# Kernel optimization log

Measured on AMD Instinct MI355X. Metric: run time of the kernel, lower is better.

The kernel has to match this reference:

```python
import jax, jax.numpy as jnp
import numpy as np

B, S, D, H = 2, 2048, 1024, 16
HD = D // H  # head dim = 64


def setup_inputs() -> dict:
    key = jax.random.key(0)
    ks = jax.random.split(key, 5)
    scale = 0.02
    x = jax.random.normal(ks[0], (B, S, D), dtype=jnp.float32)
    Wqkv = jax.random.normal(ks[1], (D, 3 * D), dtype=jnp.float32) * scale
    bqkv = jnp.zeros((3 * D,), dtype=jnp.float32)
    Wproj = jax.random.normal(ks[2], (D, D), dtype=jnp.float32) * scale
    bproj = jnp.zeros((D,), dtype=jnp.float32)
    return {"x": x, "Wqkv": Wqkv, "bqkv": bqkv, "Wproj": Wproj, "bproj": bproj}


def reference(x, Wqkv, bqkv, Wproj, bproj):
    # fused QKV projection
    qkv = x @ Wqkv + bqkv                      # [B, S, 3D]
    q, k, v = jnp.split(qkv, 3, axis=-1)       # each [B, S, D]
    # split heads -> [B, H, S, HD]
    def heads(t):
        return t.reshape(B, S, H, HD).transpose(0, 2, 1, 3)
    q, k, v = heads(q), heads(k), heads(v)
    # scaled dot-product attention with causal mask (GPT-2 style)
    scores = jnp.einsum('bhqd,bhkd->bhqk', q, k) / jnp.sqrt(jnp.float32(HD))
    causal = jnp.tril(jnp.ones((S, S), dtype=bool))
    scores = jnp.where(causal, scores, jnp.finfo(scores.dtype).min)
    attn = jax.nn.softmax(scores, axis=-1)      # [B, H, S, S]
    out = jnp.einsum('bhqk,bhkd->bhqd', attn, v)  # [B, H, S, HD]
    out = out.transpose(0, 2, 1, 3).reshape(B, S, D)
    return out @ Wproj + bproj
```

## Files before the change

kernel.cpp:

```cpp
#include <hip/hip_runtime.h>
#include <hip/hip_bf16.h>


typedef __attribute__((ext_vector_type(8))) short short8;
typedef __attribute__((ext_vector_type(4))) float float4v;

#define S_LEN 2048
#define NHEAD 16
#define HDIM  64
#define DMODEL 1024

__device__ __forceinline__ unsigned short f2bf(float f) {
    union { float f; unsigned u; } v; v.f = f;
    unsigned r = v.u + 0x7FFF + ((v.u >> 16) & 1);
    return (unsigned short)(r >> 16);
}

__device__ __forceinline__ unsigned fbits_rn(float f) {
    union { float f; unsigned u; } v; v.f = f;
    return v.u + 0x8000u;
}

__device__ __forceinline__ void async16(const void* g, const void* l) {
    __builtin_amdgcn_global_load_lds(
        (const __attribute__((address_space(1))) unsigned int*)g,
        (__attribute__((address_space(3))) unsigned int*)l, 16, 0, 0);
}

__global__ void f32_to_bf16_v4(const float4* __restrict__ in,
                               ushort4* __restrict__ out, int n4) {
    int i = blockIdx.x * blockDim.x + threadIdx.x;
    if (i < n4) {
        float4 v = in[i];
        ushort4 o;
        o.x = f2bf(v.x); o.y = f2bf(v.y); o.z = f2bf(v.z); o.w = f2bf(v.w);
        out[i] = o;
    }
}

__global__ __launch_bounds__(256) void w_transpose_bf16(
    const float* __restrict__ Wqkv, const float* __restrict__ Wproj,
    unsigned short* __restrict__ outQ, unsigned short* __restrict__ outP) {
    __shared__ float t[64][65];
    const float* in; unsigned short* out; int N, bxl;
    if (blockIdx.x < 48) { in = Wqkv;  out = outQ; N = 3072; bxl = blockIdx.x; }
    else                 { in = Wproj; out = outP; N = 1024; bxl = blockIdx.x - 48; }
    const int K = 1024;
    const int kb = blockIdx.y * 64, nb = bxl * 64;
    const int tid = threadIdx.x;
    const int r0 = tid >> 4, c0 = (tid & 15) * 4;
#pragma unroll
    for (int g = 0; g < 4; g++) {
        float4 v = *(const float4*)(in + (size_t)(kb + g * 16 + r0) * N + nb + c0);
        t[g * 16 + r0][c0 + 0] = v.x; t[g * 16 + r0][c0 + 1] = v.y;
        t[g * 16 + r0][c0 + 2] = v.z; t[g * 16 + r0][c0 + 3] = v.w;
    }
    __syncthreads();
#pragma unroll
    for (int g = 0; g < 4; g++) {
        int n = g * 16 + r0;
        ushort4 o;
        o.x = f2bf(t[c0 + 0][n]); o.y = f2bf(t[c0 + 1][n]);
        o.z = f2bf(t[c0 + 2][n]); o.w = f2bf(t[c0 + 3][n]);
        *(ushort4*)(out + (size_t)(nb + n) * K + kb + c0) = o;
    }
}

__global__ __launch_bounds__(256) void v_pack(
    const unsigned short* __restrict__ V, unsigned short* __restrict__ Vp) {
    __shared__ unsigned short t[64 * 68];
    const int bh = blockIdx.y;
    const int c0 = blockIdx.x;
    const int s0 = c0 * 64;
    const int tid = threadIdx.x;
    const int r = tid >> 2, c4 = tid & 3;
    const size_t base = (size_t)bh * S_LEN * HDIM;
    union { uint4 v[2]; unsigned short u[16]; } d;
    const unsigned short* src = V + base + (size_t)(s0 + r) * HDIM + c4 * 16;
    d.v[0] = *(const uint4*)(src);
    d.v[1] = *(const uint4*)(src + 8);
#pragma unroll
    for (int j = 0; j < 16; j++) t[r * 68 + c4 * 16 + j] = d.u[j];
    __syncthreads();
    unsigned short* outb = Vp + ((size_t)(bh * 32 + c0)) * 4096;
#pragma unroll
    for (int pi = 0; pi < 2; pi++) {
        const int p = tid * 2 + pi;
        const int lane = p & 63, kk = (p >> 6) & 1, nt = p >> 7;
        const int q = lane >> 4, l = lane & 15;
        union { ushort4 v[2]; unsigned short u[8]; } w;
#pragma unroll
        for (int j = 0; j < 8; j++) {
            const int key = (kk * 2 + (j >> 2)) * 16 + q * 4 + (j & 3);
            w.u[j] = t[key * 68 + nt * 16 + l];
        }
        unsigned short* po = outb + ((nt * 2 + kk) * 64 + lane) * 8;
        *(ushort4*)(po) = w.v[0];
        *(ushort4*)(po + 4) = w.v[1];
    }
}

#define QSCALE 0.18033688f

__global__ __launch_bounds__(256) void gemm_qkv_kernel(
    const unsigned short* __restrict__ A,
    const unsigned short* __restrict__ Bt,
    const float* __restrict__ bias,
    unsigned short* __restrict__ out_q,
    unsigned short* __restrict__ out_kp,
    unsigned short* __restrict__ out_v,
    int M, int N, int K)
{
    __shared__ unsigned short smem[128 * 132];
    unsigned short* As = smem;
    unsigned short* Bs = smem + 8192;

    const int tid  = threadIdx.x;
    const int lane = tid & 63;
    const int wave = tid >> 6;
    const int quad = lane >> 4;
    const int l16  = lane & 15;

    const int m0 = blockIdx.y * 128;
    const int n0 = blockIdx.x * 128;
    const int wm = (wave >> 1) * 64;
    const int wn = (wave & 1) * 64;

    float4v acc[4][4];
#pragma unroll
    for (int i = 0; i < 4; i++)
#pragma unroll
        for (int j = 0; j < 4; j++) acc[i][j] = (float4v){0.f, 0.f, 0.f, 0.f};

    const int srow = lane >> 2;
    const int scol = (lane & 3) * 8;

    for (int k0 = 0; k0 < K; k0 += 64) {
        __syncthreads();
#pragma unroll
        for (int kk = 0; kk < 2; kk++)
#pragma unroll
            for (int it = 0; it < 2; it++) {
                const int rg = it * 64 + wave * 16;
                async16(A  + (size_t)(m0 + rg + srow) * K + k0 + kk * 32 + scol,
                        (const char*)(As + kk * 4096) + rg * 64);
                async16(Bt + (size_t)(n0 + rg + srow) * K + k0 + kk * 32 + scol,
                        (const char*)(Bs + kk * 4096) + rg * 64);
            }
        __syncthreads();

#pragma unroll
        for (int kk = 0; kk < 2; kk++) {
            short8 af[4], bf[4];
#pragma unroll
            for (int mt = 0; mt < 4; mt++)
                af[mt] = *(const short8*)(As + kk * 4096
                                          + (wm + mt * 16 + l16) * 32 + quad * 8);
#pragma unroll
            for (int nt = 0; nt < 4; nt++)
                bf[nt] = *(const short8*)(Bs + kk * 4096
                                          + (wn + nt * 16 + l16) * 32 + quad * 8);
#pragma unroll
            for (int mt = 0; mt < 4; mt++)
#pragma unroll
                for (int nt = 0; nt < 4; nt++)
                    acc[mt][nt] = __builtin_amdgcn_mfma_f32_16x16x32_bf16(
                        af[mt], bf[nt], acc[mt][nt], 0, 0, 0);
        }
    }

    __syncthreads();
#pragma unroll
    for (int nt = 0; nt < 4; nt++) {
        const int col = n0 + wn + nt * 16 + l16;
        const float sc = ((col >> 10) == 0) ? QSCALE : 1.0f;
        const float bia = bias[col] * sc;
        const int cold = (wn + nt * 16 + l16) >> 1;
#pragma unroll
        for (int mt = 0; mt < 4; mt++)
#pragma unroll
            for (int r = 0; r < 4; r++) {
                unsigned fb = fbits_rn(acc[mt][nt][r] * sc + bia);
                unsigned fbp = (unsigned)__shfl_xor((int)fb, 1, 64);
                unsigned pd = (l16 & 1)
                    ? __builtin_amdgcn_perm(fb, fbp, 0x07060302)
                    : __builtin_amdgcn_perm(fbp, fb, 0x07060302);
                const int rowl = wm + mt * 16 + quad * 4 + r;
                *((unsigned*)smem + rowl * 66 + cold) = pd;
            }
    }
    __syncthreads();

#pragma unroll
    for (int ps = 0; ps < 8; ps++) {
        const int row = ps * 16 + (tid >> 4);
        const int pc  = tid & 15;
        const int col0 = pc * 8;
        const int cb = n0 + (col0 >> 6) * 64;
        const int part = cb >> 10;
        const int hh = (cb & 1023) >> 6;
        const int gr = m0 + row;
        const int b = gr >> 11, s = gr & 2047;
        const size_t bhI = (size_t)(b * NHEAD + hh);
        const unsigned short* pl = smem + row * 132 + col0;
        uint2 a = *(const uint2*)(pl);
        uint2 bb = *(const uint2*)(pl + 4);
        uint4 w; w.x = a.x; w.y = a.y; w.z = bb.x; w.w = bb.y;
        unsigned short* po;
        if (part == 1) {
            const int hd = col0 & 63;
            const int h = hd >> 5, q = (hd >> 3) & 3;
            po = out_kp + ((((bhI * 32 + (s >> 6)) * 4 + ((s >> 4) & 3)) * 2 + h)
                           * 64 + q * 16 + (s & 15)) * 8;
        } else {
            unsigned short* dst = (part == 0) ? out_q : out_v;
            po = dst + (bhI * S_LEN + s) * HDIM + (col0 & 63);
        }
        *(uint4*)po = w;
    }
}

__global__ __launch_bounds__(256) void gemm_proj_kernel(
    const unsigned short* __restrict__ A,
    const unsigned short* __restrict__ Bt,
    const float* __restrict__ bias,
    float* __restrict__ out_f,
    int M, int N, int K)
{
    __shared__ unsigned short smem[12288];
    unsigned short* As = smem;
    unsigned short* Bs = smem + 4096;

    const int tid  = threadIdx.x;
    const int lane = tid & 63;
    const int wave = tid >> 6;
    const int quad = lane >> 4;
    const int l16  = lane & 15;

    const int m0 = blockIdx.y * 64;
    const int n0 = blockIdx.x * 128;
    const int wm = (wave >> 1) * 32;
    const int wn = (wave & 1) * 64;

    float4v acc[2][4];
#pragma unroll
    for (int i = 0; i < 2; i++)
#pragma unroll
        for (int j = 0; j < 4; j++) acc[i][j] = (float4v){0.f, 0.f, 0.f, 0.f};

    const int srow = lane >> 2;
    const int scol = (lane & 3) * 8;

    for (int k0 = 0; k0 < K; k0 += 64) {
        __syncthreads();
#pragma unroll
        for (int kk = 0; kk < 2; kk++) {
            async16(A + (size_t)(m0 + wave * 16 + srow) * K + k0 + kk * 32 + scol,
                    (const char*)(As + kk * 2048) + wave * 1024);
#pragma unroll
            for (int it = 0; it < 2; it++) {
                const int rg = it * 64 + wave * 16;
                async16(Bt + (size_t)(n0 + rg + srow) * K + k0 + kk * 32 + scol,
                        (const char*)(Bs + kk * 4096) + rg * 64);
            }
        }
        __syncthreads();

#pragma unroll
        for (int kk = 0; kk < 2; kk++) {
            short8 af[2], bf[4];
#pragma unroll
            for (int mt = 0; mt < 2; mt++)
                af[mt] = *(const short8*)(As + kk * 2048
                                          + (wm + mt * 16 + l16) * 32 + quad * 8);
#pragma unroll
            for (int nt = 0; nt < 4; nt++)
                bf[nt] = *(const short8*)(Bs + kk * 4096
                                          + (wn + nt * 16 + l16) * 32 + quad * 8);
#pragma unroll
            for (int mt = 0; mt < 2; mt++)
#pragma unroll
                for (int nt = 0; nt < 4; nt++)
                    acc[mt][nt] = __builtin_amdgcn_mfma_f32_16x16x32_bf16(
                        af[mt], bf[nt], acc[mt][nt], 0, 0, 0);
        }
    }

#pragma unroll
    for (int nt = 0; nt < 4; nt++) {
        const int col = n0 + wn + nt * 16 + l16;
        const float bia = bias[col];
#pragma unroll
        for (int mt = 0; mt < 2; mt++) {
            const int rowb = m0 + wm + mt * 16 + quad * 4;
#pragma unroll
            for (int r = 0; r < 4; r++)
                out_f[(size_t)(rowb + r) * N + col] = acc[mt][nt][r] + bia;
        }
    }
}

__global__ __launch_bounds__(256, 2) void attn7_kernel(
    const unsigned short* __restrict__ Q,
    const unsigned short* __restrict__ Kp,
    const unsigned short* __restrict__ Vp,
    unsigned short* __restrict__ ctx)
{
    __shared__ unsigned short lds[2][8192];

    const int tid  = threadIdx.x;
    const int lane = tid & 63;
    const int wave = tid >> 6;
    const int quad = lane >> 4;
    const int l16  = lane & 15;

    const int bx = blockIdx.x;
    const int bh = bx & 31;
    const int g  = bx >> 5;
    const int qb = (g < 8) ? (15 - g) : (g - 8);
    const int q0w = qb * 128 + wave * 32;
    const int nch = 2 * qb + 2;

    const size_t baseQ = (size_t)bh * S_LEN * HDIM;
    const unsigned short* kb_ = Kp + (size_t)bh * 32 * 4096;
    const unsigned short* vb_ = Vp + (size_t)bh * 32 * 4096;

    short8 qf[2][2];
#pragma unroll
    for (int qt = 0; qt < 2; qt++)
#pragma unroll
        for (int h = 0; h < 2; h++)
            qf[qt][h] = *(const short8*)(Q + baseQ
                                         + (size_t)(q0w + qt * 16 + l16) * HDIM
                                         + h * 32 + quad * 8);

    float4v o[2][4];
#pragma unroll
    for (int qt = 0; qt < 2; qt++)
#pragma unroll
        for (int nt = 0; nt < 4; nt++) o[qt][nt] = (float4v){0.f, 0.f, 0.f, 0.f};
    float lsa[2][4];
#pragma unroll
    for (int qt = 0; qt < 2; qt++)
#pragma unroll
        for (int kt = 0; kt < 4; kt++) lsa[qt][kt] = 0.f;

    {
        unsigned short* sb = &lds[0][0];
        async16(kb_ + tid * 8,        sb + wave * 512);
        async16(kb_ + 2048 + tid * 8, sb + 2048 + wave * 512);
        async16(vb_ + tid * 8,        sb + 4096 + wave * 512);
        async16(vb_ + 2048 + tid * 8, sb + 6144 + wave * 512);
    }

    for (int c = 0; c < nch; c++) {
        __syncthreads();
        const unsigned short* lb = &lds[c & 1][0];
        const int kb0 = c * 64;
        const bool wactive = (kb0 <= q0w + 31);

        short8 kf[4][2];
        if (wactive) {
#pragma unroll
            for (int kt = 0; kt < 4; kt++)
#pragma unroll
                for (int h = 0; h < 2; h++)
                    kf[kt][h] = *(const short8*)(lb
                                                 + ((kt * 2 + h) * 64 + lane) * 8);
        }

        if (c + 1 < nch) {
            const unsigned short* kc = kb_ + (size_t)(c + 1) * 4096;
            const unsigned short* vc = vb_ + (size_t)(c + 1) * 4096;
            unsigned short* sb = &lds[(c + 1) & 1][0];
            async16(kc + tid * 8,        sb + wave * 512);
            async16(kc + 2048 + tid * 8, sb + 2048 + wave * 512);
            async16(vc + tid * 8,        sb + 4096 + wave * 512);
            async16(vc + 2048 + tid * 8, sb + 6144 + wave * 512);
        }

        if (wactive) {
            float4v st[2][4];
#pragma unroll
            for (int qt = 0; qt < 2; qt++)
#pragma unroll
                for (int kt = 0; kt < 4; kt++) {
                    st[qt][kt] = __builtin_amdgcn_mfma_f32_16x16x32_bf16(
                        kf[kt][0], qf[qt][0], (float4v){0.f, 0.f, 0.f, 0.f},
                        0, 0, 0);
                    st[qt][kt] = __builtin_amdgcn_mfma_f32_16x16x32_bf16(
                        kf[kt][1], qf[qt][1], st[qt][kt], 0, 0, 0);
                }

            short8 vf[4][2];
#pragma unroll
            for (int nt = 0; nt < 4; nt++)
#pragma unroll
                for (int kk = 0; kk < 2; kk++)
                    vf[nt][kk] = *(const short8*)(lb + 4096
                                                  + ((nt * 2 + kk) * 64 + lane) * 8);

#pragma unroll
            for (int qt = 0; qt < 2; qt++) {
                const int q0t = q0w + qt * 16;
                const bool needmask = (kb0 + 63 > q0t);
                const int qpos = q0t + l16;
                float p[4][4];
#pragma unroll
                for (int kt = 0; kt < 4; kt++)
#pragma unroll
                    for (int r = 0; r < 4; r++) {
                        float x = st[qt][kt][r];
                        if (needmask) {
                            int kpos = kb0 + kt * 16 + quad * 4 + r;
                            x = (kpos <= qpos) ? x : -1e30f;
                        }
                        p[kt][r] = __builtin_amdgcn_exp2f(x);
                        lsa[qt][kt] += p[kt][r];
                    }

                unsigned pk[4][2];
#pragma unroll
                for (int kt = 0; kt < 4; kt++)
#pragma unroll
                    for (int j = 0; j < 2; j++)
                        pk[kt][j] = __builtin_amdgcn_perm(
                            fbits_rn(p[kt][2 * j + 1]), fbits_rn(p[kt][2 * j]),
                            0x07060302);
                union { unsigned u[4]; short8 s; } pf[2];
#pragma unroll
                for (int kk = 0; kk < 2; kk++)
#pragma unroll
                    for (int pp = 0; pp < 4; pp++)
                        pf[kk].u[pp] = pk[kk * 2 + (pp >> 1)][pp & 1];

#pragma unroll
                for (int nt = 0; nt < 4; nt++) {
                    o[qt][nt] = __builtin_amdgcn_mfma_f32_16x16x32_bf16(
                        pf[0].s, vf[nt][0], o[qt][nt], 0, 0, 0);
                    o[qt][nt] = __builtin_amdgcn_mfma_f32_16x16x32_bf16(
                        pf[1].s, vf[nt][1], o[qt][nt], 0, 0, 0);
                }
            }
        }
    }

    const int b = bh >> 4, h = bh & 15;
#pragma unroll
    for (int qt = 0; qt < 2; qt++) {
        float l = (lsa[qt][0] + lsa[qt][1]) + (lsa[qt][2] + lsa[qt][3]);
        l += __shfl_xor(l, 16, 64);
        l += __shfl_xor(l, 32, 64);
        const float linv = 1.f / l;
        float lr[4];
#pragma unroll
        for (int r = 0; r < 4; r++) lr[r] = __shfl(linv, quad * 4 + r, 64);
#pragma unroll
        for (int r = 0; r < 4; r++) {
            const int s = q0w + qt * 16 + quad * 4 + r;
            const size_t off = ((size_t)(b * S_LEN + s)) * DMODEL + h * HDIM;
#pragma unroll
            for (int nt = 0; nt < 4; nt++)
                ctx[off + nt * 16 + l16] = f2bf(o[qt][nt][r] * lr[r]);
        }
    }
}

extern "C" void kernel_launch(void* const* d_in, const int* in_sizes, int n_in,
                              void* d_out, int out_size, void* d_ws, size_t ws_size,
                              hipStream_t stream) {
    const float* x     = (const float*)d_in[0];
    const float* Wqkv  = (const float*)d_in[1];
    const float* bqkv  = (const float*)d_in[2];
    const float* Wproj = (const float*)d_in[3];
    const float* bproj = (const float*)d_in[4];
    float* out = (float*)d_out;

    const int M  = 2 * S_LEN;
    const int N1 = 3 * DMODEL;
    const int K  = DMODEL;

    unsigned short* x_bf    = (unsigned short*)d_ws;
    unsigned short* wqkv_t  = x_bf   + (size_t)M * K;
    unsigned short* wproj_t = wqkv_t + (size_t)K * N1;
    unsigned short* q_bf    = wproj_t + (size_t)K * DMODEL;
    unsigned short* kp_bf   = q_bf   + (size_t)M * DMODEL;
    unsigned short* v_bf    = kp_bf  + (size_t)M * DMODEL;
    unsigned short* ctx_bf  = v_bf   + (size_t)M * DMODEL;
    unsigned short* vp_bf   = x_bf;

    {
        int n4 = (M * K) / 4;
        f32_to_bf16_v4<<<n4 / 256, 256, 0, stream>>>((const float4*)x,
                                                     (ushort4*)x_bf, n4);
    }
    {
        dim3 g(64, 16);
        w_transpose_bf16<<<g, 256, 0, stream>>>(Wqkv, Wproj, wqkv_t, wproj_t);
    }

    dim3 g1(N1 / 128, M / 128);
    gemm_qkv_kernel<<<g1, 256, 0, stream>>>(x_bf, wqkv_t, bqkv,
                                            q_bf, kp_bf, v_bf, M, N1, K);

    {
        dim3 g(S_LEN / 64, 2 * NHEAD);
        v_pack<<<g, 256, 0, stream>>>(v_bf, vp_bf);
    }

    attn7_kernel<<<512, 256, 0, stream>>>(q_bf, kp_bf, vp_bf, ctx_bf);

    dim3 g3(DMODEL / 128, M / 64);
    gemm_proj_kernel<<<g3, 256, 0, stream>>>(ctx_bf, wproj_t, bproj, out,
                                             M, DMODEL, K);
}
```

Measured before the change: 184.1 us.

## Halve attention block to 64 queries with 2 waves and 1024 blocks

The attention kernel now uses 128-thread blocks covering 64 query rows instead of 256 threads covering 128, and launches twice as many blocks. Each K/V chunk is loaded by fewer threads in four iterations, and the per-wave causal skip is removed because every wave now works on every chunk up to the diagonal. This cuts the idle waves and load imbalance along the causal diagonal and spreads work across more blocks. In exchange, each K/V tile is reused by only two waves, so total LDS fill traffic roughly doubles.

```diff
diff --git a/kernel.cpp b/kernel.cpp
--- a/kernel.cpp
+++ b/kernel.cpp
@@ -300,7 +300,7 @@
     }
 }
 
-__global__ __launch_bounds__(256, 2) void attn7_kernel(
+__global__ __launch_bounds__(128, 2) void attn8_kernel(
     const unsigned short* __restrict__ Q,
     const unsigned short* __restrict__ Kp,
     const unsigned short* __restrict__ Vp,
@@ -317,9 +317,13 @@
     const int bx = blockIdx.x;
     const int bh = bx & 31;
     const int g  = bx >> 5;
-    const int qb = (g < 8) ? (15 - g) : (g - 8);
-    const int q0w = qb * 128 + wave * 32;
-    const int nch = 2 * qb + 2;
+    const int g0 = g & 7, gt = g >> 3;
+    const int qb = (gt == 0) ? (31 - g0)
+                 : (gt == 1) ? (16 + g0)
+                 : (gt == 2) ? (15 - g0)
+                 :             g0;
+    const int q0w = qb * 64 + wave * 32;
+    const int nch = qb + 1;
 
     const size_t baseQ = (size_t)bh * S_LEN * HDIM;
     const unsigned short* kb_ = Kp + (size_t)bh * 32 * 4096;
@@ -347,100 +351,100 @@
 
     {
         unsigned short* sb = &lds[0][0];
-        async16(kb_ + tid * 8,        sb + wave * 512);
-        async16(kb_ + 2048 + tid * 8, sb + 2048 + wave * 512);
-        async16(vb_ + tid * 8,        sb + 4096 + wave * 512);
-        async16(vb_ + 2048 + tid * 8, sb + 6144 + wave * 512);
+#pragma unroll
+        for (int i = 0; i < 4; i++) {
+            async16(kb_ + (size_t)(i * 128 + tid) * 8,
+                    sb + (i * 128 + wave * 64) * 8);
+            async16(vb_ + (size_t)(i * 128 + tid) * 8,
+                    sb + 4096 + (i * 128 + wave * 64) * 8);
+        }
     }
 
     for (int c = 0; c < nch; c++) {
         __syncthreads();
         const unsigned short* lb = &lds[c & 1][0];
         const int kb0 = c * 64;
-        const bool wactive = (kb0 <= q0w + 31);
 
         short8 kf[4][2];
-        if (wactive) {
-#pragma unroll
-            for (int kt = 0; kt < 4; kt++)
-#pragma unroll
-                for (int h = 0; h < 2; h++)
-                    kf[kt][h] = *(const short8*)(lb
-                                                 + ((kt * 2 + h) * 64 + lane) * 8);
-        }
+#pragma unroll
+        for (int kt = 0; kt < 4; kt++)
+#pragma unroll
+            for (int h = 0; h < 2; h++)
+                kf[kt][h] = *(const short8*)(lb + ((kt * 2 + h) * 64 + lane) * 8);
 
         if (c + 1 < nch) {
             const unsigned short* kc = kb_ + (size_t)(c + 1) * 4096;
             const unsigned short* vc = vb_ + (size_t)(c + 1) * 4096;
             unsigned short* sb = &lds[(c + 1) & 1][0];
-            async16(kc + tid * 8,        sb + wave * 512);
-            async16(kc + 2048 + tid * 8, sb + 2048 + wave * 512);
-            async16(vc + tid * 8,        sb + 4096 + wave * 512);
-            async16(vc + 2048 + tid * 8, sb + 6144 + wave * 512);
-        }
-
-        if (wactive) {
-            float4v st[2][4];
-#pragma unroll
-            for (int qt = 0; qt < 2; qt++)
-#pragma unroll
-                for (int kt = 0; kt < 4; kt++) {
-                    st[qt][kt] = __builtin_amdgcn_mfma_f32_16x16x32_bf16(
-                        kf[kt][0], qf[qt][0], (float4v){0.f, 0.f, 0.f, 0.f},
-                        0, 0, 0);
-                    st[qt][kt] = __builtin_amdgcn_mfma_f32_16x16x32_bf16(
-                        kf[kt][1], qf[qt][1], st[qt][kt], 0, 0, 0);
+#pragma unroll
+            for (int i = 0; i < 4; i++) {
+                async16(kc + (size_t)(i * 128 + tid) * 8,
+                        sb + (i * 128 + wave * 64) * 8);
+                async16(vc + (size_t)(i * 128 + tid) * 8,
+                        sb + 4096 + (i * 128 + wave * 64) * 8);
+            }
+        }
+
+        float4v st[2][4];
+#pragma unroll
+        for (int qt = 0; qt < 2; qt++)
+#pragma unroll
+            for (int kt = 0; kt < 4; kt++) {
+                st[qt][kt] = __builtin_amdgcn_mfma_f32_16x16x32_bf16(
+                    kf[kt][0], qf[qt][0], (float4v){0.f, 0.f, 0.f, 0.f},
+                    0, 0, 0);
+                st[qt][kt] = __builtin_amdgcn_mfma_f32_16x16x32_bf16(
+                    kf[kt][1], qf[qt][1], st[qt][kt], 0, 0, 0);
+            }
+
+        short8 vf[4][2];
+#pragma unroll
+        for (int nt = 0; nt < 4; nt++)
+#pragma unroll
+            for (int kk = 0; kk < 2; kk++)
+                vf[nt][kk] = *(const short8*)(lb + 4096
+                                              + ((nt * 2 + kk) * 64 + lane) * 8);
+
+#pragma unroll
+        for (int qt = 0; qt < 2; qt++) {
+            const int q0t = q0w + qt * 16;
+            const bool needmask = (kb0 + 63 > q0t);
+            const int qpos = q0t + l16;
+            float p[4][4];
+#pragma unroll
+            for (int kt = 0; kt < 4; kt++)
+#pragma unroll
+                for (int r = 0; r < 4; r++) {
+                    float x = st[qt][kt][r];
+                    if (needmask) {
+                        int kpos = kb0 + kt * 16 + quad * 4 + r;
+                        x = (kpos <= qpos) ? x : -1e30f;
+                    }
+                    p[kt][r] = __builtin_amdgcn_exp2f(x);
+                    lsa[qt][kt] += p[kt][r];
                 }
 
-            short8 vf[4][2];
-#pragma unroll
-            for (int nt = 0; nt < 4; nt++)
-#pragma unroll
-                for (int kk = 0; kk < 2; kk++)
-                    vf[nt][kk] = *(const short8*)(lb + 4096
-                                                  + ((nt * 2 + kk) * 64 + lane) * 8);
-
-#pragma unroll
-            for (int qt = 0; qt < 2; qt++) {
-                const int q0t = q0w + qt * 16;
-                const bool needmask = (kb0 + 63 > q0t);
-                const int qpos = q0t + l16;
-                float p[4][4];
-#pragma unroll
-                for (int kt = 0; kt < 4; kt++)
-#pragma unroll
-                    for (int r = 0; r < 4; r++) {
-                        float x = st[qt][kt][r];
-                        if (needmask) {
-                            int kpos = kb0 + kt * 16 + quad * 4 + r;
-                            x = (kpos <= qpos) ? x : -1e30f;
-                        }
-                        p[kt][r] = __builtin_amdgcn_exp2f(x);
-                        lsa[qt][kt] += p[kt][r];
-                    }
-
-                unsigned pk[4][2];
-#pragma unroll
-                for (int kt = 0; kt < 4; kt++)
-#pragma unroll
-                    for (int j = 0; j < 2; j++)
-                        pk[kt][j] = __builtin_amdgcn_perm(
-                            fbits_rn(p[kt][2 * j + 1]), fbits_rn(p[kt][2 * j]),
-                            0x07060302);
-                union { unsigned u[4]; short8 s; } pf[2];
-#pragma unroll
-                for (int kk = 0; kk < 2; kk++)
-#pragma unroll
-                    for (int pp = 0; pp < 4; pp++)
-                        pf[kk].u[pp] = pk[kk * 2 + (pp >> 1)][pp & 1];
-
-#pragma unroll
-                for (int nt = 0; nt < 4; nt++) {
-                    o[qt][nt] = __builtin_amdgcn_mfma_f32_16x16x32_bf16(
-                        pf[0].s, vf[nt][0], o[qt][nt], 0, 0, 0);
-                    o[qt][nt] = __builtin_amdgcn_mfma_f32_16x16x32_bf16(
-                        pf[1].s, vf[nt][1], o[qt][nt], 0, 0, 0);
-                }
+            unsigned pk[4][2];
+#pragma unroll
+            for (int kt = 0; kt < 4; kt++)
+#pragma unroll
+                for (int j = 0; j < 2; j++)
+                    pk[kt][j] = __builtin_amdgcn_perm(
+                        fbits_rn(p[kt][2 * j + 1]), fbits_rn(p[kt][2 * j]),
+                        0x07060302);
+            union { unsigned u[4]; short8 s; } pf[2];
+#pragma unroll
+            for (int kk = 0; kk < 2; kk++)
+#pragma unroll
+                for (int pp = 0; pp < 4; pp++)
+                    pf[kk].u[pp] = pk[kk * 2 + (pp >> 1)][pp & 1];
+
+#pragma unroll
+            for (int nt = 0; nt < 4; nt++) {
+                o[qt][nt] = __builtin_amdgcn_mfma_f32_16x16x32_bf16(
+                    pf[0].s, vf[nt][0], o[qt][nt], 0, 0, 0);
+                o[qt][nt] = __builtin_amdgcn_mfma_f32_16x16x32_bf16(
+                    pf[1].s, vf[nt][1], o[qt][nt], 0, 0, 0);
             }
         }
     }
@@ -508,7 +512,7 @@
         v_pack<<<g, 256, 0, stream>>>(v_bf, vp_bf);
     }
 
-    attn7_kernel<<<512, 256, 0, stream>>>(q_bf, kp_bf, vp_bf, ctx_bf);
+    attn8_kernel<<<1024, 128, 0, stream>>>(q_bf, kp_bf, vp_bf, ctx_bf);
 
     dim3 g3(DMODEL / 128, M / 64);
     gemm_proj_kernel<<<g3, 256, 0, stream>>>(ctx_bf, wproj_t, bproj, out,
```

New measurement: 186.0 us. No clear change (+1.0%).
